# Performance work log

Hardware: AMD Instinct MI355X
Metric: run time of the kernel (lower is better)

The kernel has to match this reference:

```python
import jax, jax.numpy as jnp
import numpy as np

N = 100_000   # nodes
E = 3_200_000 # edges (avg degree 32)
F_NODE = 64
F_EDGE = 16
HID = 64
NEG_SLOPE = 0.2


def _gat_conv(x, src, dst, edge_attr, W, a_src, a_dst, We, a_e, bias, n):
    """PyG GATConv (heads=1, edge_dim, add_self_loops=True fill='mean', eval mode)."""
    # --- add self loops; loop edge_attr = mean of incoming edge_attr per node ---
    deg = jax.ops.segment_sum(jnp.ones((src.shape[0],), x.dtype), dst, num_segments=n)
    loop_attr = jax.ops.segment_sum(edge_attr, dst, num_segments=n)
    loop_attr = jnp.where(deg[:, None] > 0, loop_attr / jnp.maximum(deg, 1.0)[:, None], 0.0)
    loop = jnp.arange(n, dtype=src.dtype)
    src2 = jnp.concatenate([src, loop])
    dst2 = jnp.concatenate([dst, loop])
    ea = jnp.concatenate([edge_attr, loop_attr], axis=0)

    # --- node / edge projections and per-node attention terms ---
    h = x @ W                                   # [N, HID]
    alpha_src = h @ a_src                       # [N]
    alpha_dst = h @ a_dst                       # [N]
    e = ea @ We                                 # [E+N, HID]
    alpha_e = e @ a_e                           # [E+N]

    # --- per-edge logits + segment softmax over destination neighborhoods ---
    logits = jax.nn.leaky_relu(alpha_src[src2] + alpha_dst[dst2] + alpha_e, NEG_SLOPE)
    seg_max = jax.ops.segment_max(logits, dst2, num_segments=n)  # every node has self loop
    ex = jnp.exp(logits - seg_max[dst2])
    denom = jax.ops.segment_sum(ex, dst2, num_segments=n)
    w = ex / denom[dst2]                        # [E+N]

    # --- weighted scatter-aggregate of messages ---
    out = jax.ops.segment_sum(h[src2] * w[:, None], dst2, num_segments=n)
    return out + bias


def setup_inputs() -> dict:
    key = jax.random.key(0)
    ks = jax.random.split(key, 16)
    s = 0.1  # keep logits tame
    return {
        "x": jax.random.normal(ks[0], (N, F_NODE), jnp.float32),
        "edge_index": jax.random.randint(ks[1], (2, E), 0, N, jnp.int32),
        "edge_attr": jax.random.normal(ks[2], (E, F_EDGE), jnp.float32),
        "W1": jax.random.normal(ks[3], (F_NODE, HID), jnp.float32) * s,
        "att_src1": jax.random.normal(ks[4], (HID,), jnp.float32) * s,
        "att_dst1": jax.random.normal(ks[5], (HID,), jnp.float32) * s,
        "We1": jax.random.normal(ks[6], (F_EDGE, HID), jnp.float32) * s,
        "att_edge1": jax.random.normal(ks[7], (HID,), jnp.float32) * s,
        "b1": jnp.zeros((HID,), jnp.float32),
        "W2": jax.random.normal(ks[8], (HID, HID), jnp.float32) * s,
        "att_src2": jax.random.normal(ks[9], (HID,), jnp.float32) * s,
        "att_dst2": jax.random.normal(ks[10], (HID,), jnp.float32) * s,
        "We2": jax.random.normal(ks[11], (F_EDGE, HID), jnp.float32) * s,
        "att_edge2": jax.random.normal(ks[12], (HID,), jnp.float32) * s,
        "b2": jnp.zeros((HID,), jnp.float32),
        "fc_w": jax.random.normal(ks[13], (HID, 1), jnp.float32) * s,
        "fc_b": jnp.zeros((1,), jnp.float32),
    }


def reference(x, edge_index, edge_attr, W1, att_src1, att_dst1, We1, att_edge1, b1,
              W2, att_src2, att_dst2, We2, att_edge2, b2, fc_w, fc_b):
    src, dst = edge_index[0], edge_index[1]
    n = x.shape[0]
    h = jax.nn.elu(_gat_conv(x, src, dst, edge_attr, W1, att_src1, att_dst1, We1, att_edge1, b1, n))
    h = jax.nn.elu(_gat_conv(h, src, dst, edge_attr, W2, att_src2, att_dst2, We2, att_edge2, b2, n))
    return h @ fc_w + fc_b  # [N, 1] logits
```

## Files before the change

kernel.cpp:

```cpp
#include <hip/hip_runtime.h>
#include <hip/hip_bf16.h>
#include <hip/hip_fp16.h>
#include <math.h>
#include <stdint.h>

constexpr int HIDDIM = 64;
constexpr int FEDGE  = 16;
constexpr int BN     = 256;
constexpr int CAP    = 9216;
constexpr int TILE   = 2048;
constexpr int NTA    = 512;
constexpr int EPT    = TILE / NTA;

__global__ void compute_c_kernel(const float* __restrict__ We1, const float* __restrict__ ae1,
                                 const float* __restrict__ We2, const float* __restrict__ ae2,
                                 float* __restrict__ c) {
  int t = threadIdx.x;
  if (t < FEDGE) {
    float s = 0.f;
    for (int j = 0; j < HIDDIM; ++j) s += We1[t * HIDDIM + j] * ae1[j];
    c[t] = s;
  } else if (t < 2 * FEDGE) {
    int k = t - FEDGE;
    float s = 0.f;
    for (int j = 0; j < HIDDIM; ++j) s += We2[k * HIDDIM + j] * ae2[j];
    c[FEDGE + k] = s;
  }
}

__device__ __forceinline__ int pack_ae(float a1, float a2) {
  unsigned lo = __half_as_ushort(__float2half_rn(a1));
  unsigned hi = __half_as_ushort(__float2half_rn(a2));
  return (int)((hi << 16) | lo);
}
template <int SEL>
__device__ __forceinline__ float unpack_ae(int pk) {
  unsigned u = (SEL == 0) ? ((unsigned)pk & 0xFFFFu) : ((unsigned)pk >> 16);
  return __half2float(__ushort_as_half((unsigned short)u));
}

__global__ __launch_bounds__(NTA) void passA_kernel(
    const int* __restrict__ src, const int* __restrict__ dst,
    const float* __restrict__ attr, const float* __restrict__ c,
    int* __restrict__ bucketCursor, int2* __restrict__ P, int E, int nbuck) {
  __shared__ int st_ae[TILE];
  __shared__ int s_key[TILE];
  __shared__ int s_ae[TILE];
  __shared__ int s_b[TILE];
  __shared__ int cnt[400];
  __shared__ int lbase[512];
  __shared__ int gbase[400];
  __shared__ float cs[32];
  if (threadIdx.x < 32) cs[threadIdx.x] = c[threadIdx.x];
  for (int i = threadIdx.x; i < nbuck; i += NTA) cnt[i] = 0;
  __syncthreads();
  int e0 = blockIdx.x * TILE;
  int tileCnt = min(TILE, E - e0);

  int d_reg[EPT];
#pragma unroll
  for (int k = 0; k < EPT; ++k) {
    int e = e0 + k * NTA + threadIdx.x;
    d_reg[k] = (e < E) ? dst[e] : -1;
  }
#pragma unroll
  for (int k = 0; k < EPT; ++k) {
    if (d_reg[k] >= 0) atomicAdd(&cnt[d_reg[k] >> 8], 1);
  }

  {
    int q   = threadIdx.x & 3;
    int grp = threadIdx.x >> 2;
    const float4* attr4 = (const float4*)attr;
#pragma unroll
    for (int pass = 0; pass < TILE / 128; ++pass) {
      int el = pass * 128 + grp;
      int e = e0 + el;
      float4 v = make_float4(0.f, 0.f, 0.f, 0.f);
      if (e < E) v = attr4[(size_t)e * 4 + q];
      float a1 = v.x * cs[4*q]    + v.y * cs[4*q+1]    + v.z * cs[4*q+2]    + v.w * cs[4*q+3];
      float a2 = v.x * cs[16+4*q] + v.y * cs[16+4*q+1] + v.z * cs[16+4*q+2] + v.w * cs[16+4*q+3];
      a1 += __shfl_xor(a1, 1, 64); a1 += __shfl_xor(a1, 2, 64);
      a2 += __shfl_xor(a2, 1, 64); a2 += __shfl_xor(a2, 2, 64);
      if (q == 0) st_ae[el] = pack_ae(a1, a2);
    }
  }
  __syncthreads();

  {
    int t = threadIdx.x;
    int v = (t < nbuck) ? cnt[t] : 0;
    lbase[t] = v;
    __syncthreads();
    for (int d = 1; d < 512; d <<= 1) {
      int tv = (t >= d) ? lbase[t - d] : 0;
      __syncthreads();
      lbase[t] += tv;
      __syncthreads();
    }
    lbase[t] -= v;
  }
  for (int i = threadIdx.x; i < nbuck; i += NTA) {
    int n = cnt[i];
    gbase[i] = (n > 0) ? atomicAdd(&bucketCursor[i], n) : 0;
    cnt[i] = 0;
  }
  __syncthreads();

#pragma unroll
  for (int k = 0; k < EPT; ++k) {
    int d = d_reg[k];
    if (d < 0) continue;
    int el = k * NTA + threadIdx.x;
    int e = e0 + el;
    int b = d >> 8;
    int sE = src[e];
    int r = atomicAdd(&cnt[b], 1);
    int idx = lbase[b] + r;
    s_key[idx] = sE | ((d & 255) << 20);
    s_ae[idx]  = st_ae[el];
    s_b[idx]   = b;
  }
  __syncthreads();

  for (int i = threadIdx.x; i < tileCnt; i += NTA) {
    int b = s_b[i];
    int rank = i - lbase[b];
    int pos = gbase[b] + rank;
    if (pos < CAP) P[(size_t)b * CAP + pos] = make_int2(s_key[i], s_ae[i]);
  }
}

__global__ void scan_buckets_kernel(const int* __restrict__ bucketCursor,
                                    int* __restrict__ bucketBase,
                                    int* __restrict__ offsets, int nbuck, int N, int E) {
  __shared__ int s[512];
  int t = threadIdx.x;
  int v = (t < nbuck) ? min(bucketCursor[t], CAP) : 0;
  s[t] = v;
  __syncthreads();
  for (int d = 1; d < 512; d <<= 1) {
    int tv = (t >= d) ? s[t - d] : 0;
    __syncthreads();
    s[t] += tv;
    __syncthreads();
  }
  if (t < nbuck) bucketBase[t] = s[t] - v;
  if (t == 0) offsets[N] = E;
}

__global__ __launch_bounds__(256) void passB_kernel(
    const int2* __restrict__ P, const int* __restrict__ bucketCursor,
    const int* __restrict__ bucketBase, int* __restrict__ offsets,
    int2* __restrict__ EDGS, int N) {
  int b = blockIdx.x;
  int t = threadIdx.x;
  int nodeBase = b * BN;
  int cnt = min(bucketCursor[b], CAP);
  int gbase = bucketBase[b];
  __shared__ int hist[BN];
  __shared__ int cur[BN];
  __shared__ int wsum[4];
  hist[t] = 0;
  __syncthreads();
  const int2* Pb = P + (size_t)b * CAP;
  for (int i = t; i < cnt; i += 256) {
    int dl = (Pb[i].x >> 20) & 255;
    atomicAdd(&hist[dl], 1);
  }
  __syncthreads();
  int deg = hist[t];
  int lane = t & 63, wid = t >> 6;
  int incl = deg;
#pragma unroll
  for (int d = 1; d < 64; d <<= 1) {
    int tv = __shfl_up(incl, d, 64);
    if (lane >= d) incl += tv;
  }
  if (lane == 63) wsum[wid] = incl;
  __syncthreads();
  int woff = 0;
  for (int w = 0; w < wid; ++w) woff += wsum[w];
  int excl = incl - deg + woff;
  int nodeId = nodeBase + t;
  if (nodeId < N) offsets[nodeId] = gbase + excl;
  cur[t] = gbase + excl;
  __syncthreads();
  for (int i = t; i < cnt; i += 256) {
    int2 r = Pb[i];
    int dl = (r.x >> 20) & 255;
    int pos = atomicAdd(&cur[dl], 1);
    EDGS[pos] = r;
  }
}

__global__ __launch_bounds__(256) void gemm_alpha_kernel(
    const float* __restrict__ X, const float* __restrict__ W,
    const float* __restrict__ a_src, const float* __restrict__ a_dst,
    __half2* __restrict__ H, float* __restrict__ alpha_s, float* __restrict__ alpha_d, int n) {
  __shared__ float Ws[HIDDIM * HIDDIM];
  __shared__ float as_s[HIDDIM], ad_s[HIDDIM];
  for (int i = threadIdx.x; i < HIDDIM * HIDDIM; i += blockDim.x) Ws[i] = W[i];
  if (threadIdx.x < HIDDIM) {
    as_s[threadIdx.x] = a_src[threadIdx.x];
    ad_s[threadIdx.x] = a_dst[threadIdx.x];
  }
  __syncthreads();
  int lane = threadIdx.x & 63;
  int wid  = threadIdx.x >> 6;
  int wavesTotal = (blockDim.x >> 6) * gridDim.x;
  for (int row = blockIdx.x * (blockDim.x >> 6) + wid; row < n; row += wavesTotal) {
    float xv = X[(size_t)row * HIDDIM + lane];
    float acc = 0.f;
#pragma unroll
    for (int k = 0; k < HIDDIM; ++k) {
      float xk = __shfl(xv, k, 64);
      acc = fmaf(xk, Ws[k * HIDDIM + lane], acc);
    }
    float accN = __shfl_xor(acc, 1, 64);
    if (!(lane & 1)) {
      H[(size_t)row * 32 + (lane >> 1)] = __floats2half2_rn(acc, accN);
    }
    float s1 = acc * as_s[lane];
    float s2 = acc * ad_s[lane];
#pragma unroll
    for (int d = 32; d > 0; d >>= 1) {
      s1 += __shfl_xor(s1, d, 64);
      s2 += __shfl_xor(s2, d, 64);
    }
    if (lane == 0) {
      alpha_s[row] = s1;
      alpha_d[row] = s2;
    }
  }
}

__device__ __forceinline__ float leaky(float x) { return (x < 0.f) ? 0.2f * x : x; }
__device__ __forceinline__ float elu(float x) { return (x > 0.f) ? x : (__expf(x) - 1.f); }

template <bool FINAL, int SEL>
__global__ __launch_bounds__(256) void aggregate_kernel(
    const __half2* __restrict__ H, const float* __restrict__ alpha_s, const float* __restrict__ alpha_d,
    const int2* __restrict__ EDGS, const int* __restrict__ offsets,
    const float* __restrict__ bias, const float* __restrict__ fc_w, const float* __restrict__ fc_b,
    float* __restrict__ out, int n) {
  int lane = threadIdx.x & 63;
  int wid  = threadIdx.x >> 6;
  int node = blockIdx.x * (blockDim.x >> 6) + wid;
  if (node >= n) return;
  int off = offsets[node];
  int deg = offsets[node + 1] - off;
  float ad  = alpha_d[node];
  float asn = alpha_s[node];

  if (deg <= 64) {
    int2 ed = make_int2(0, 0);
    if (lane < deg) ed = EDGS[off + lane];
    int   s_l  = ed.x & 0xFFFFF;
    float ae_l = unpack_ae<SEL>(ed.y);
    float as_g = (lane < deg) ? alpha_s[s_l] : 0.f;
    float lg_l = (lane < deg) ? leaky(as_g + ad + ae_l) : -INFINITY;
    float aesum = (lane < deg) ? ae_l : 0.f;
    float lmax = lg_l;
#pragma unroll
    for (int d = 32; d > 0; d >>= 1) {
      lmax = fmaxf(lmax, __shfl_xor(lmax, d, 64));
      aesum += __shfl_xor(aesum, d, 64);
    }
    float self_ae = (deg > 0) ? aesum / (float)deg : 0.f;
    float slg = leaky(asn + ad + self_ae);
    float m = fmaxf(lmax, slg);

    float ex_l = (lane < deg) ? __expf(lg_l - m) : 0.f;
    float dsum = ex_l;
#pragma unroll
    for (int d = 32; d > 0; d >>= 1) dsum += __shfl_xor(dsum, d, 64);
    float exs = __expf(slg - m);
    float denom = dsum + exs;

    int half = lane >> 5;
    int c32  = lane & 31;

    float selfw = (half == 0) ? exs : 0.f;
    float2 hv = __half22float2(H[(size_t)node * 32 + c32]);
    float2 acc2;
    acc2.x = selfw * hv.x;
    acc2.y = selfw * hv.y;

    int jj = 0;
    for (; jj + 16 <= deg; jj += 16) {
      int   si[8]; float ei[8];
#pragma unroll
      for (int k = 0; k < 8; ++k) {
        si[k] = __shfl(s_l, jj + 2 * k + half, 64);
        ei[k] = __shfl(ex_l, jj + 2 * k + half, 64);
      }
      float2 hh[8];
#pragma unroll
      for (int k = 0; k < 8; ++k) hh[k] = __half22float2(H[(size_t)si[k] * 32 + c32]);
#pragma unroll
      for (int k = 0; k < 8; ++k) {
        acc2.x = fmaf(ei[k], hh[k].x, acc2.x);
        acc2.y = fmaf(ei[k], hh[k].y, acc2.y);
      }
    }
    for (; jj + 8 <= deg; jj += 8) {
      int j0 = jj + half, j1 = jj + 2 + half, j2 = jj + 4 + half, j3 = jj + 6 + half;
      int   sa = __shfl(s_l, j0, 64),  sb = __shfl(s_l, j1, 64);
      int   sc = __shfl(s_l, j2, 64),  sd = __shfl(s_l, j3, 64);
      float ea = __shfl(ex_l, j0, 64), eb = __shfl(ex_l, j1, 64);
      float ec = __shfl(ex_l, j2, 64), ef = __shfl(ex_l, j3, 64);
      float2 ha = __half22float2(H[(size_t)sa * 32 + c32]);
      float2 hb = __half22float2(H[(size_t)sb * 32 + c32]);
      float2 hc = __half22float2(H[(size_t)sc * 32 + c32]);
      float2 hd = __half22float2(H[(size_t)sd * 32 + c32]);
      acc2.x = fmaf(ea, ha.x, acc2.x); acc2.y = fmaf(ea, ha.y, acc2.y);
      acc2.x = fmaf(eb, hb.x, acc2.x); acc2.y = fmaf(eb, hb.y, acc2.y);
      acc2.x = fmaf(ec, hc.x, acc2.x); acc2.y = fmaf(ec, hc.y, acc2.y);
      acc2.x = fmaf(ef, hd.x, acc2.x); acc2.y = fmaf(ef, hd.y, acc2.y);
    }
    for (; jj < deg; jj += 2) {
      int j = jj + half;
      int   sj = __shfl(s_l, j, 64);
      float ej = __shfl(ex_l, j, 64);
      float2 hj = __half22float2(H[(size_t)sj * 32 + c32]);
      acc2.x = fmaf(ej, hj.x, acc2.x);
      acc2.y = fmaf(ej, hj.y, acc2.y);
    }
    acc2.x += __shfl_xor(acc2.x, 32, 64);
    acc2.y += __shfl_xor(acc2.y, 32, 64);

    const float2* bi2 = (const float2*)bias;
    float2 bv = bi2[c32];
    float rx = elu(acc2.x / denom + bv.x);
    float ry = elu(acc2.y / denom + bv.y);
    if (!FINAL) {
      if (half == 0) {
        float2 o; o.x = rx; o.y = ry;
        ((float2*)out)[(size_t)node * 32 + c32] = o;
      }
    } else {
      const float2* fw2 = (const float2*)fc_w;
      float2 fv = fw2[c32];
      float s1 = rx * fv.x + ry * fv.y;
#pragma unroll
      for (int d = 16; d > 0; d >>= 1) s1 += __shfl_xor(s1, d, 64);
      if (lane == 0) out[node] = s1 + fc_b[0];
    }
    return;
  }

  {
    const __half* Hh = (const __half*)H;
    float lmax = -INFINITY, aesum = 0.f;
    for (int base = 0; base < deg; base += 64) {
      int i = base + lane;
      if (i < deg) {
        int2 ed = EDGS[off + i];
        int s = ed.x & 0xFFFFF;
        float ae = unpack_ae<SEL>(ed.y);
        float lg = leaky(alpha_s[s] + ad + ae);
        lmax = fmaxf(lmax, lg);
        aesum += ae;
      }
    }
#pragma unroll
    for (int d = 32; d > 0; d >>= 1) {
      lmax = fmaxf(lmax, __shfl_xor(lmax, d, 64));
      aesum += __shfl_xor(aesum, d, 64);
    }
    float self_ae = aesum / (float)deg;
    float slg = leaky(asn + ad + self_ae);
    float m = fmaxf(lmax, slg);
    float exs = __expf(slg - m);
    float dsum = 0.f;
    float acc = exs * __half2float(Hh[(size_t)node * HIDDIM + lane]);
    for (int base = 0; base < deg; base += 64) {
      int i = base + lane;
      int cnt = min(64, deg - base);
      int2 ed = make_int2(0, 0);
      if (i < deg) ed = EDGS[off + i];
      int   s_l  = ed.x & 0xFFFFF;
      float ae_l = unpack_ae<SEL>(ed.y);
      float ex_l = (lane < cnt) ? __expf(leaky(alpha_s[s_l] + ad + ae_l) - m) : 0.f;
      dsum += ex_l;
      for (int j = 0; j < cnt; ++j) {
        int   sj = __shfl(s_l, j, 64);
        float ej = __shfl(ex_l, j, 64);
        acc = fmaf(ej, __half2float(Hh[(size_t)sj * HIDDIM + lane]), acc);
      }
    }
#pragma unroll
    for (int d = 32; d > 0; d >>= 1) dsum += __shfl_xor(dsum, d, 64);
    float denom = dsum + exs;

    float res = elu(acc / denom + bias[lane]);
    if (!FINAL) {
      out[(size_t)node * HIDDIM + lane] = res;
    } else {
      float s1 = res * fc_w[lane];
#pragma unroll
      for (int d = 32; d > 0; d >>= 1) s1 += __shfl_xor(s1, d, 64);
      if (lane == 0) out[node] = s1 + fc_b[0];
    }
  }
}

extern "C" void kernel_launch(void* const* d_in, const int* in_sizes, int n_in,
                              void* d_out, int out_size, void* d_ws, size_t ws_size,
                              hipStream_t stream) {
  const float* x    = (const float*)d_in[0];
  const int*   ei   = (const int*)d_in[1];
  const float* attr = (const float*)d_in[2];
  const float* W1   = (const float*)d_in[3];
  const float* as1  = (const float*)d_in[4];
  const float* ad1  = (const float*)d_in[5];
  const float* We1  = (const float*)d_in[6];
  const float* ae1  = (const float*)d_in[7];
  const float* b1   = (const float*)d_in[8];
  const float* W2   = (const float*)d_in[9];
  const float* as2  = (const float*)d_in[10];
  const float* ad2  = (const float*)d_in[11];
  const float* We2  = (const float*)d_in[12];
  const float* ae2  = (const float*)d_in[13];
  const float* b2   = (const float*)d_in[14];
  const float* fcw  = (const float*)d_in[15];
  const float* fcb  = (const float*)d_in[16];

  const int N = in_sizes[0] / HIDDIM;
  const int E = in_sizes[1] / 2;
  const int NBUCK = (N + BN - 1) / BN;

  char* p = (char*)d_ws;
  auto alloc = [&](size_t bytes) -> void* {
    void* r = (void*)p;
    p += (bytes + 255) & ~(size_t)255;
    return r;
  };
  float*  c            = (float*)alloc(32 * sizeof(float));
  int*    bucketCursor = (int*)alloc((size_t)NBUCK * 4);
  int*    bucketBase   = (int*)alloc(((size_t)NBUCK + 1) * 4);
  int*    offsets      = (int*)alloc(((size_t)N + 1) * 4);
  float*  alpha_s      = (float*)alloc((size_t)N * 4);
  float*  alpha_d      = (float*)alloc((size_t)N * 4);
  int2*   EDGS         = (int2*)alloc((size_t)E * 8);
  size_t  regionBytes  = (size_t)NBUCK * CAP * 8;
  size_t  hBytes       = (size_t)N * HIDDIM * 2;
  size_t  x2Bytes      = (size_t)N * HIDDIM * 4;
  if (hBytes + x2Bytes > regionBytes) regionBytes = hBytes + x2Bytes;
  char*   region       = (char*)alloc(regionBytes);
  int2*   P            = (int2*)region;
  __half2* H           = (__half2*)region;
  float*  X2           = (float*)(region + ((hBytes + 255) & ~(size_t)255));

  const int* srcp = ei;
  const int* dstp = ei + E;

  hipMemsetAsync(bucketCursor, 0, (size_t)NBUCK * 4, stream);

  compute_c_kernel<<<1, 64, 0, stream>>>(We1, ae1, We2, ae2, c);

  int ablocks = (E + TILE - 1) / TILE;
  passA_kernel<<<ablocks, NTA, 0, stream>>>(srcp, dstp, attr, c, bucketCursor, P, E, NBUCK);
  scan_buckets_kernel<<<1, 512, 0, stream>>>(bucketCursor, bucketBase, offsets, NBUCK, N, E);
  passB_kernel<<<NBUCK, 256, 0, stream>>>(P, bucketCursor, bucketBase, offsets, EDGS, N);

  int aggBlocks = (N + 3) / 4;

  gemm_alpha_kernel<<<2048, 256, 0, stream>>>(x, W1, as1, ad1, H, alpha_s, alpha_d, N);
  aggregate_kernel<false, 0><<<aggBlocks, 256, 0, stream>>>(H, alpha_s, alpha_d, EDGS,
                                                            offsets, b1, nullptr, nullptr, X2, N);
  gemm_alpha_kernel<<<2048, 256, 0, stream>>>(X2, W2, as2, ad2, H, alpha_s, alpha_d, N);
  aggregate_kernel<true, 1><<<aggBlocks, 256, 0, stream>>>(H, alpha_s, alpha_d, EDGS,
                                                           offsets, b2, fcw, fcb, (float*)d_out, N);
}
```

Before: 449.9 us.

## Use wave-shuffle bucket scan in passA and unroll aggregation gathers by 32

Replaces passA's 512-wide shared-memory Hillis-Steele scan, which needs about 18 barriers, with a wavefront shuffle scan plus a cross-wave sum. The global bucket-cursor atomics are now issued before the edge-attribute projection so their latency can overlap it. The aggregate kernel gains a 32-edge unrolled gather loop to keep more H loads in flight per wave, at the cost of extra registers and possibly lower occupancy. The bucketCursor buffer is padded to 512 entries so every thread can index it safely.

Result: slower. 466.5 us (+3.7%).

```diff
diff --git a/kernel.cpp b/kernel.cpp
--- a/kernel.cpp
+++ b/kernel.cpp
@@ -49,10 +49,12 @@
   __shared__ int s_b[TILE];
   __shared__ int cnt[400];
   __shared__ int lbase[512];
-  __shared__ int gbase[400];
+  __shared__ int gbase[512];
+  __shared__ int wsum[8];
   __shared__ float cs[32];
-  if (threadIdx.x < 32) cs[threadIdx.x] = c[threadIdx.x];
-  for (int i = threadIdx.x; i < nbuck; i += NTA) cnt[i] = 0;
+  int t = threadIdx.x;
+  if (t < 32) cs[t] = c[t];
+  for (int i = t; i < nbuck; i += NTA) cnt[i] = 0;
   __syncthreads();
   int e0 = blockIdx.x * TILE;
   int tileCnt = min(TILE, E - e0);
@@ -60,17 +62,38 @@
   int d_reg[EPT];
 #pragma unroll
   for (int k = 0; k < EPT; ++k) {
-    int e = e0 + k * NTA + threadIdx.x;
+    int e = e0 + k * NTA + t;
     d_reg[k] = (e < E) ? dst[e] : -1;
   }
 #pragma unroll
   for (int k = 0; k < EPT; ++k) {
     if (d_reg[k] >= 0) atomicAdd(&cnt[d_reg[k] >> 8], 1);
   }
-
+  __syncthreads();
+
+  int lane = t & 63, w = t >> 6;
+  int n = (t < nbuck) ? cnt[t] : 0;
+  int ret = 0;
+  if (n > 0) ret = atomicAdd(&bucketCursor[t], n);
+  int incl = n;
+#pragma unroll
+  for (int d = 1; d < 64; d <<= 1) {
+    int tv = __shfl_up(incl, d, 64);
+    if (lane >= d) incl += tv;
+  }
+  if (lane == 63) wsum[w] = incl;
+  __syncthreads();
   {
-    int q   = threadIdx.x & 3;
-    int grp = threadIdx.x >> 2;
+    int woff = 0;
+#pragma unroll
+    for (int w2 = 0; w2 < 8; ++w2) woff += (w2 < w) ? wsum[w2] : 0;
+    lbase[t] = incl - n + woff;
+    if (t < nbuck) cnt[t] = 0;
+  }
+
+  {
+    int q   = t & 3;
+    int grp = t >> 2;
     const float4* attr4 = (const float4*)attr;
 #pragma unroll
     for (int pass = 0; pass < TILE / 128; ++pass) {
@@ -85,33 +108,14 @@
       if (q == 0) st_ae[el] = pack_ae(a1, a2);
     }
   }
-  __syncthreads();
-
-  {
-    int t = threadIdx.x;
-    int v = (t < nbuck) ? cnt[t] : 0;
-    lbase[t] = v;
-    __syncthreads();
-    for (int d = 1; d < 512; d <<= 1) {
-      int tv = (t >= d) ? lbase[t - d] : 0;
-      __syncthreads();
-      lbase[t] += tv;
-      __syncthreads();
-    }
-    lbase[t] -= v;
-  }
-  for (int i = threadIdx.x; i < nbuck; i += NTA) {
-    int n = cnt[i];
-    gbase[i] = (n > 0) ? atomicAdd(&bucketCursor[i], n) : 0;
-    cnt[i] = 0;
-  }
+  gbase[t] = ret;
   __syncthreads();
 
 #pragma unroll
   for (int k = 0; k < EPT; ++k) {
     int d = d_reg[k];
     if (d < 0) continue;
-    int el = k * NTA + threadIdx.x;
+    int el = k * NTA + t;
     int e = e0 + el;
     int b = d >> 8;
     int sE = src[e];
@@ -123,7 +127,7 @@
   }
   __syncthreads();
 
-  for (int i = threadIdx.x; i < tileCnt; i += NTA) {
+  for (int i = t; i < tileCnt; i += NTA) {
     int b = s_b[i];
     int rank = i - lbase[b];
     int pos = gbase[b] + rank;
@@ -288,6 +292,22 @@
     acc2.y = selfw * hv.y;
 
     int jj = 0;
+    for (; jj + 32 <= deg; jj += 32) {
+      int   si[16]; float ei[16];
+#pragma unroll
+      for (int k = 0; k < 16; ++k) {
+        si[k] = __shfl(s_l, jj + 2 * k + half, 64);
+        ei[k] = __shfl(ex_l, jj + 2 * k + half, 64);
+      }
+      float2 hh[16];
+#pragma unroll
+      for (int k = 0; k < 16; ++k) hh[k] = __half22float2(H[(size_t)si[k] * 32 + c32]);
+#pragma unroll
+      for (int k = 0; k < 16; ++k) {
+        acc2.x = fmaf(ei[k], hh[k].x, acc2.x);
+        acc2.y = fmaf(ei[k], hh[k].y, acc2.y);
+      }
+    }
     for (; jj + 16 <= deg; jj += 16) {
       int   si[8]; float ei[8];
 #pragma unroll
@@ -438,7 +458,7 @@
     return r;
   };
   float*  c            = (float*)alloc(32 * sizeof(float));
-  int*    bucketCursor = (int*)alloc((size_t)NBUCK * 4);
+  int*    bucketCursor = (int*)alloc(512 * 4);
   int*    bucketBase   = (int*)alloc(((size_t)NBUCK + 1) * 4);
   int*    offsets      = (int*)alloc(((size_t)N + 1) * 4);
   float*  alpha_s      = (float*)alloc((size_t)N * 4);
@@ -456,7 +476,7 @@
   const int* srcp = ei;
   const int* dstp = ei + E;
 
-  hipMemsetAsync(bucketCursor, 0, (size_t)NBUCK * 4, stream);
+  hipMemsetAsync(bucketCursor, 0, 512 * 4, stream);
 
   compute_c_kernel<<<1, 64, 0, stream>>>(We1, ae1, We2, ae2, c);
 
```
